# Performance work log

Hardware: AMD Instinct MI355X
Metric: run time of the kernel (lower is better)

The kernel has to match this reference:

```python
import jax, jax.numpy as jnp
import numpy as np

NUM_CENTROIDS = 64
NUM_KMEANS = 5
KM_ITERS = 20


def _kmeans_labels(X, key):
    """Lloyd k-means on X [N,D]; returns final cluster labels [N] (int32).
    Mirrors faiss.Kmeans(dim, num_centroids, niter=...) label assignment."""
    N, D = X.shape
    idx = jax.random.choice(key, N, (NUM_CENTROIDS,), replace=False)
    cent0 = X[idx]  # [C,D] init from random data points

    def assign(cent):
        d = (cent * cent).sum(-1)[None, :] - 2.0 * (X @ cent.T)  # [N,C]
        return jnp.argmin(d, axis=1)

    def step(cent, _):
        lab = assign(cent)
        sums = jax.ops.segment_sum(X, lab, num_segments=NUM_CENTROIDS)  # [C,D]
        cnts = jax.ops.segment_sum(jnp.ones((N,), X.dtype), lab, num_segments=NUM_CENTROIDS)
        newc = jnp.where(cnts[:, None] > 0, sums / jnp.maximum(cnts, 1.0)[:, None], cent)
        return newc, None

    cent, _ = jax.lax.scan(step, cent0, None, length=KM_ITERS)
    return assign(cent)


def setup_inputs() -> dict:
    key = jax.random.key(0)
    k1, k2, k3 = jax.random.split(key, 3)
    N, D = 8192, 512
    adj = jax.random.uniform(k1, (N, N), dtype=jnp.float32)
    student = jax.random.normal(k2, (N, D), dtype=jnp.float32)
    teacher = jax.random.normal(k3, (N, D), dtype=jnp.float32)
    return {"adj": adj, "student": student, "teacher": teacher, "topk": 16}


def reference(adj, student, teacher, topk):
    N, D = student.shape
    # similarity = (student @ teacher.T).detach() + 10*I
    sim = jax.lax.stop_gradient(student @ teacher.T) + 10.0 * jnp.eye(N, dtype=student.dtype)
    _, I_knn = jax.lax.top_k(sim, topk)  # [N, k], sorted descending
    rows = jnp.arange(N)[:, None]  # [N,1]

    # knn_neighbor: sparse ones at (row, I_knn); topk cols are distinct per row
    knn_pat = jnp.zeros((N, N), adj.dtype).at[rows, I_knn].set(1.0)
    locality = knn_pat * adj  # sparse elementwise product knn_neighbor * adj

    # k-means cluster labels over NUM_KMEANS seeds (teacher is detached/cpu in torch)
    Xt = jax.lax.stop_gradient(teacher)
    keys = jax.random.split(jax.random.key(1234), NUM_KMEANS)
    labels = jax.vmap(lambda k: _kmeans_labels(Xt, k))(keys)  # [M,N]

    # close-in-background mask: any seed where label(i) == label(knn_j(i))
    ngh_lab = labels[:, I_knn]               # [M,N,k]
    mask = jnp.any(labels[:, :, None] == ngh_lab, axis=0)  # [N,k]

    # globality: ones at masked (row, knn) positions
    glob_pat = jnp.zeros((N, N), adj.dtype).at[rows, I_knn].add(mask.astype(adj.dtype))

    # pos = locality + globality (dense equivalent of coalesced sparse sum)
    pos = locality + glob_pat
    return pos
```

## Files before the change

kernel.cpp:

```cpp
#include <hip/hip_runtime.h>
#include <stdint.h>

typedef unsigned int u32;
typedef unsigned long long u64;
typedef __attribute__((ext_vector_type(8))) short short8;
typedef __attribute__((ext_vector_type(4))) float f32x4;

#define NN 8192
#define DD 512
#define CC 64
#define RR 5
#define KM_ITERS 20
#define TOPKK 16
#define CHUNK 4096
#define GAP_TH 0.05f
#define FLAGTH 0.02f
#define BAND_TH 0.01f

#define MFMA_BF16 __builtin_amdgcn_mfma_f32_16x16x32_bf16

__device__ __forceinline__ void gload16(void* lds, const void* g) {
  __builtin_amdgcn_global_load_lds(
      (const __attribute__((address_space(1))) void*)g,
      (__attribute__((address_space(3))) void*)lds, 16, 0, 0);
}

__device__ __forceinline__ void tf2x32(u32 k0, u32 k1, u32 x0, u32 x1,
                                       u32& o0, u32& o1) {
  u32 ks2 = k0 ^ k1 ^ 0x1BD11BDAu;
  x0 += k0; x1 += k1;
#define TFR(r) { x0 += x1; x1 = (x1 << r) | (x1 >> (32 - r)); x1 ^= x0; }
  TFR(13) TFR(15) TFR(26) TFR(6)
  x0 += k1; x1 += ks2 + 1u;
  TFR(17) TFR(29) TFR(16) TFR(24)
  x0 += ks2; x1 += k0 + 2u;
  TFR(13) TFR(15) TFR(26) TFR(6)
  x0 += k0; x1 += k1 + 3u;
  TFR(17) TFR(29) TFR(16) TFR(24)
  x0 += k1; x1 += ks2 + 4u;
  TFR(13) TFR(15) TFR(26) TFR(6)
  x0 += ks2; x1 += k0 + 5u;
#undef TFR
  o0 = x0; o1 = x1;
}

__global__ __launch_bounds__(256) void rng_kernel(u32* __restrict__ bits1,
                                                  u32* __restrict__ bits2) {
  int r = blockIdx.x;
  int i = blockIdx.y * 256 + threadIdx.x;
  u32 rk0, rk1; tf2x32(0u, 1234u, 0u, (u32)r, rk0, rk1);
  u32 k10, k11, s10, s11, s20, s21;
  tf2x32(rk0, rk1, 0u, 0u, k10, k11);
  tf2x32(rk0, rk1, 0u, 1u, s10, s11);
  tf2x32(k10, k11, 0u, 1u, s20, s21);
  u32 a, b;
  tf2x32(s10, s11, 0u, (u32)i, a, b);
  bits1[r * NN + i] = a ^ b;
  tf2x32(s20, s21, 0u, (u32)i, a, b);
  bits2[r * NN + i] = a ^ b;
}

__global__ __launch_bounds__(256) void rankpart_kernel(const u32* __restrict__ bits,
                                                       u32* __restrict__ prank) {
  __shared__ u64 sk[2048];
  int r = blockIdx.x, zc = blockIdx.z;
  const u32* bb = bits + (size_t)r * NN;
  int jbase = zc * 2048;
  for (int t = threadIdx.x; t < 2048; t += 256)
    sk[t] = ((u64)bb[jbase + t] << 13) | (u32)(jbase + t);
  __syncthreads();
  int i = blockIdx.y * 256 + threadIdx.x;
  u64 ki = ((u64)bb[i] << 13) | (u32)i;
  int cnt = 0;
#pragma unroll 8
  for (int j = 0; j < 2048; ++j) cnt += (int)(sk[j] < ki);
  prank[(size_t)(r * 4 + zc) * NN + i] = cnt;
}

__global__ __launch_bounds__(256) void scat1_kernel(const u32* __restrict__ prank,
                                                    int* __restrict__ vout) {
  int r = blockIdx.x;
  int i = blockIdx.y * 256 + threadIdx.x;
  int rank = prank[(size_t)(r * 4 + 0) * NN + i] + prank[(size_t)(r * 4 + 1) * NN + i] +
             prank[(size_t)(r * 4 + 2) * NN + i] + prank[(size_t)(r * 4 + 3) * NN + i];
  vout[(size_t)r * NN + rank] = i;
}

__global__ __launch_bounds__(256) void scat2_kernel(const u32* __restrict__ prank,
                                                    const int* __restrict__ v1,
                                                    int* __restrict__ sel) {
  int r = blockIdx.x;
  int i = blockIdx.y * 256 + threadIdx.x;
  int rank = prank[(size_t)(r * 4 + 0) * NN + i] + prank[(size_t)(r * 4 + 1) * NN + i] +
             prank[(size_t)(r * 4 + 2) * NN + i] + prank[(size_t)(r * 4 + 3) * NN + i];
  if (rank < CC) sel[r * CC + rank] = v1[(size_t)r * NN + i];
}

__device__ __forceinline__ double block_reduce_d(double s, double* red4) {
  int tid = threadIdx.x;
  for (int off = 32; off > 0; off >>= 1) s += __shfl_down(s, off, 64);
  if ((tid & 63) == 0) red4[tid >> 6] = s;
  __syncthreads();
  return red4[0] + red4[1] + red4[2] + red4[3];
}

__device__ __forceinline__ u32 bf16rne(float a) {
  u32 ab = __float_as_uint(a);
  return (ab + 0x7FFFu + ((ab >> 16) & 1u)) >> 16;
}
__device__ __forceinline__ void splitf(float a, unsigned short& hi, unsigned short& lo) {
  u32 h = bf16rne(a);
  float hf = __uint_as_float(h << 16);
  hi = (unsigned short)h;
  lo = (unsigned short)bf16rne(a - hf);
}

__global__ __launch_bounds__(256) void init_cent_kernel(const float* __restrict__ X,
                                                        const int* __restrict__ sel,
                                                        double* __restrict__ centD,
                                                        double* __restrict__ cnD,
                                                        float* __restrict__ cnF,
                                                        unsigned short* __restrict__ CHg,
                                                        unsigned short* __restrict__ CLg) {
  __shared__ double red4[4];
  int r = blockIdx.x, c = blockIdx.y, t = threadIdx.x;
  int src = sel[r * CC + c];
  const float* xp = X + (size_t)src * DD;
  size_t o = (size_t)(r * CC + c) * DD;
  double va = (double)xp[t], vb = (double)xp[t + 256];
  centD[o + t] = va; centD[o + t + 256] = vb;
  unsigned short h0, l0, h1, l1;
  splitf((float)va, h0, l0); splitf((float)vb, h1, l1);
  CHg[o + t] = h0; CLg[o + t] = l0;
  CHg[o + t + 256] = h1; CLg[o + t + 256] = l1;
  double tot = block_reduce_d(va * va + vb * vb, red4);
  if (t == 0) { cnD[r * CC + c] = tot; cnF[r * CC + c] = (float)tot; }
}

__global__ __launch_bounds__(256) void split_kernel(const float* __restrict__ in,
                                                    unsigned short* __restrict__ hi,
                                                    unsigned short* __restrict__ lo) {
  size_t base = ((size_t)blockIdx.x * 256 + threadIdx.x) * 8;
  float4 v0 = *(const float4*)(in + base);
  float4 v1 = *(const float4*)(in + base + 4);
  float vv[8] = {v0.x, v0.y, v0.z, v0.w, v1.x, v1.y, v1.z, v1.w};
  unsigned short h[8], l[8];
#pragma unroll
  for (int j = 0; j < 8; ++j) splitf(vv[j], h[j], l[j]);
  uint4 hv, lv;
  hv.x = h[0] | ((u32)h[1] << 16); hv.y = h[2] | ((u32)h[3] << 16);
  hv.z = h[4] | ((u32)h[5] << 16); hv.w = h[6] | ((u32)h[7] << 16);
  lv.x = l[0] | ((u32)l[1] << 16); lv.y = l[2] | ((u32)l[3] << 16);
  lv.z = l[4] | ((u32)l[5] << 16); lv.w = l[6] | ((u32)l[7] << 16);
  *(uint4*)(hi + base) = hv;
  *(uint4*)(lo + base) = lv;
}

__global__ __launch_bounds__(256) void assign_kernel(const unsigned short* __restrict__ XH,
                                                     const unsigned short* __restrict__ XL,
                                                     const unsigned short* __restrict__ CHg,
                                                     const unsigned short* __restrict__ CLg,
                                                     const float* __restrict__ cnF,
                                                     const float* __restrict__ Xf,
                                                     const double* __restrict__ centD,
                                                     const double* __restrict__ cnD,
                                                     int* __restrict__ labels,
                                                     int* __restrict__ bhist,
                                                     int* __restrict__ rib) {
  __shared__ unsigned short Xh[2 * 64 * 32], Xl[2 * 64 * 32],
                            Ch[2 * 64 * 32], Cl[2 * 64 * 32];
  __shared__ float dmat[64 * 68];
  __shared__ int labs[64];
  __shared__ int flagged[64];
  __shared__ int nflag;
  __shared__ double darr[CC];
  __shared__ int h[CC];
  int r = blockIdx.y;
  int blk = blockIdx.x;
  int rowBase = blk * 64;
  int tid = threadIdx.x;
  int wid = tid >> 6, lane = tid & 63, m = lane & 15, q = lane >> 4;
  int srow = wid * 16 + (lane >> 2);
  int sslot = (lane & 3) * 8;
  const unsigned short* gxh = XH + (size_t)(rowBase + srow) * DD + sslot;
  const unsigned short* gxl = XL + (size_t)(rowBase + srow) * DD + sslot;
  const unsigned short* gch = CHg + ((size_t)r * CC + srow) * DD + sslot;
  const unsigned short* gcl = CLg + ((size_t)r * CC + srow) * DD + sslot;
  f32x4 acc[4] = {};
  for (int kc = 0; kc < DD; kc += 64) {
#pragma unroll
    for (int p = 0; p < 2; ++p) {
      int off = p * 2048, ko = kc + p * 32;
      gload16(&Xh[off + wid * 512], gxh + ko);
      gload16(&Xl[off + wid * 512], gxl + ko);
      gload16(&Ch[off + wid * 512], gch + ko);
      gload16(&Cl[off + wid * 512], gcl + ko);
    }
    __syncthreads();
#pragma unroll
    for (int s = 0; s < 2; ++s) {
      int off = s * 2048;
      short8 ah = *(short8*)&Xh[off + (wid * 16 + m) * 32 + q * 8];
      short8 al = *(short8*)&Xl[off + (wid * 16 + m) * 32 + q * 8];
#pragma unroll
      for (int nt = 0; nt < 4; ++nt) {
        short8 bh = *(short8*)&Ch[off + (nt * 16 + m) * 32 + q * 8];
        short8 bl = *(short8*)&Cl[off + (nt * 16 + m) * 32 + q * 8];
        acc[nt] = MFMA_BF16(ah, bh, acc[nt], 0, 0, 0);
        acc[nt] = MFMA_BF16(ah, bl, acc[nt], 0, 0, 0);
        acc[nt] = MFMA_BF16(al, bh, acc[nt], 0, 0, 0);
      }
    }
    __syncthreads();
  }
#pragma unroll
  for (int nt = 0; nt < 4; ++nt) {
    float cn = cnF[r * CC + nt * 16 + m];
#pragma unroll
    for (int reg = 0; reg < 4; ++reg)
      dmat[(wid * 16 + q * 4 + reg) * 68 + nt * 16 + m] = cn - 2.0f * acc[nt][reg];
  }
  if (tid == 0) nflag = 0;
  if (tid < CC) h[tid] = 0;
  __syncthreads();
  if (tid < 64) {
    const float* dr = dmat + (size_t)tid * 68;
    float best = dr[0], second = 3.4e38f; int bi = 0;
    for (int c = 1; c < CC; ++c) {
      float v = dr[c];
      if (v < best) { second = best; best = v; bi = c; }
      else if (v < second) second = v;
    }
    labs[tid] = bi;
    if (second - best < GAP_TH) {
      int s = atomicAdd(&nflag, 1);
      flagged[s] = tid;
    }
  }
  __syncthreads();
  int nf = nflag;
  int cc0 = tid >> 2, sub = tid & 3;
  for (int f = 0; f < nf; ++f) {
    int row = flagged[f];
    const float* x = Xf + (size_t)(rowBase + row) * DD + sub * 128;
    const double* cp = centD + (size_t)(r * CC + cc0) * DD + sub * 128;
    double s = 0.0;
    for (int k = 0; k < 128; ++k) s += (double)x[k] * cp[k];
    s += __shfl_down(s, 2, 64);
    s += __shfl_down(s, 1, 64);
    if (sub == 0) darr[cc0] = cnD[r * CC + cc0] - 2.0 * s;
    __syncthreads();
    if (tid == 0) {
      double best = darr[0]; int bi = 0;
      for (int c2 = 1; c2 < CC; ++c2) { double v = darr[c2]; if (v < best) { best = v; bi = c2; } }
      labs[row] = bi;
    }
    __syncthreads();
  }
  if (tid < 64) {
    int lab = labs[tid];
    atomicAdd(&h[lab], 1);
    int rk = 0;
    for (int j = 0; j < tid; ++j) rk += (labs[j] == lab);
    rib[(size_t)r * NN + rowBase + tid] = rk;
    labels[(size_t)r * NN + rowBase + tid] = lab;
  }
  __syncthreads();
  if (tid < CC) bhist[(size_t)(r * 128 + blk) * CC + tid] = h[tid];
}

__global__ __launch_bounds__(256) void fill_kernel(const int* __restrict__ labels,
                                                   const int* __restrict__ rib,
                                                   const int* __restrict__ bhist,
                                                   int* __restrict__ cstart,
                                                   int* __restrict__ cnt,
                                                   int* __restrict__ member) {
  __shared__ int bh[128 * CC];
  __shared__ int cs[CC];
  __shared__ int tots[CC];
  int r = blockIdx.x, blk = blockIdx.y, tid = threadIdx.x;
  const int* src = bhist + (size_t)r * 128 * CC;
  for (int t = tid; t < 128 * CC; t += 256) bh[t] = src[t];
  __syncthreads();
  if (tid < CC) {
    int run = 0;
    for (int b = 0; b < 128; ++b) { int v = bh[b * CC + tid]; bh[b * CC + tid] = run; run += v; }
    tots[tid] = run;
  }
  __syncthreads();
  if (tid == 0) {
    int run = 0;
    for (int q2 = 0; q2 < CC; ++q2) { cs[q2] = run; run += tots[q2]; }
  }
  __syncthreads();
  int i = blk * 256 + tid;
  int lab = labels[(size_t)r * NN + i];
  int pos = cs[lab] + bh[(i >> 6) * CC + lab] + rib[(size_t)r * NN + i];
  member[(size_t)r * NN + pos] = i;
  if (blk == 0 && tid < CC) { cnt[r * CC + tid] = tots[tid]; cstart[r * CC + tid] = cs[tid]; }
}

__global__ __launch_bounds__(256) void update_kernel(const float* __restrict__ X,
                                                     const int* __restrict__ member,
                                                     const int* __restrict__ cstart,
                                                     const int* __restrict__ cnt,
                                                     const double* __restrict__ centOld,
                                                     double* __restrict__ centNew) {
  __shared__ double part[4][64];
  int r = blockIdx.x, c = blockIdx.y, dchunk = blockIdx.z;
  int tid = threadIdx.x;
  int d = dchunk * 64 + (tid & 63);
  int lane = tid >> 6;
  int n = cnt[r * CC + c];
  int st = cstart[r * CC + c];
  const int* mem = member + (size_t)r * NN + st;
  int n4 = (n + 3) >> 2;
  int lo = lane * n4;
  int hi = min(n, lo + n4);
  double s0 = 0, s1 = 0, s2 = 0, s3 = 0;
  int m = lo;
  for (; m + 3 < hi; m += 4) {
    s0 += (double)X[(size_t)mem[m + 0] * DD + d];
    s1 += (double)X[(size_t)mem[m + 1] * DD + d];
    s2 += (double)X[(size_t)mem[m + 2] * DD + d];
    s3 += (double)X[(size_t)mem[m + 3] * DD + d];
  }
  for (; m < hi; ++m) s0 += (double)X[(size_t)mem[m] * DD + d];
  part[lane][tid & 63] = (s0 + s1) + (s2 + s3);
  __syncthreads();
  if (tid < 64) {
    double tot = (part[0][tid] + part[1][tid]) + (part[2][tid] + part[3][tid]);
    size_t o = (size_t)(r * CC + c) * DD + dchunk * 64 + tid;
    double va = (n > 0) ? tot / (double)n : centOld[o];
    centNew[o] = va;
  }
}

__global__ __launch_bounds__(256) void norm_kernel(const double* __restrict__ centNew,
                                                   double* __restrict__ cnD,
                                                   float* __restrict__ cnF,
                                                   unsigned short* __restrict__ CHg,
                                                   unsigned short* __restrict__ CLg) {
  __shared__ double red4[4];
  int r = blockIdx.x, c = blockIdx.y, t = threadIdx.x;
  size_t o = (size_t)(r * CC + c) * DD;
  double va = centNew[o + t], vb = centNew[o + t + 256];
  unsigned short h0, l0, h1, l1;
  splitf((float)va, h0, l0); splitf((float)vb, h1, l1);
  CHg[o + t] = h0; CLg[o + t] = l0;
  CHg[o + t + 256] = h1; CLg[o + t + 256] = l1;
  double tot = block_reduce_d(va * va + vb * vb, red4);
  if (t == 0) { cnD[r * CC + c] = tot; cnF[r * CC + c] = (float)tot; }
}

__global__ __launch_bounds__(256) void gemm_kernel(const unsigned short* __restrict__ SH,
                                                   const unsigned short* __restrict__ SL,
                                                   const unsigned short* __restrict__ TH,
                                                   const unsigned short* __restrict__ TL,
                                                   float* __restrict__ sim,
                                                   int rowChunk) {
  __shared__ unsigned short Ah[2 * 128 * 32], Al[2 * 128 * 32],
                            Bh[2 * 128 * 32], Bl[2 * 128 * 32];
  int tid = threadIdx.x;
  int wid = tid >> 6, lane = tid & 63, m = lane & 15, q = lane >> 4;
  int waveM = wid >> 1, waveN = wid & 1;
  const int nwgx = NN / 128;
  const int nwg = nwgx * (CHUNK / 128);
  int wg = blockIdx.y * nwgx + blockIdx.x;
  int swz = (wg & 7) * (nwg >> 3) + (wg >> 3);
  int rowTile = swz / nwgx, colTile = swz % nwgx;
  int rowBase = rowChunk + rowTile * 128;
  int colBase = colTile * 128;
  int sr0 = wid * 16 + (lane >> 2);
  int sr1 = (wid + 4) * 16 + (lane >> 2);
  int sslot = (lane & 3) * 8;
  const unsigned short* gah0 = SH + (size_t)(rowBase + sr0) * DD + sslot;
  const unsigned short* gah1 = SH + (size_t)(rowBase + sr1) * DD + sslot;
  const unsigned short* gal0 = SL + (size_t)(rowBase + sr0) * DD + sslot;
  const unsigned short* gal1 = SL + (size_t)(rowBase + sr1) * DD + sslot;
  const unsigned short* gbh0 = TH + (size_t)(colBase + sr0) * DD + sslot;
  const unsigned short* gbh1 = TH + (size_t)(colBase + sr1) * DD + sslot;
  const unsigned short* gbl0 = TL + (size_t)(colBase + sr0) * DD + sslot;
  const unsigned short* gbl1 = TL + (size_t)(colBase + sr1) * DD + sslot;
  f32x4 acc[4][4] = {};
  for (int kc = 0; kc < DD; kc += 64) {
#pragma unroll
    for (int p = 0; p < 2; ++p) {
      int off = p * 4096, ko = kc + p * 32;
      gload16(&Ah[off + wid * 512], gah0 + ko);
      gload16(&Ah[off + (wid + 4) * 512], gah1 + ko);
      gload16(&Al[off + wid * 512], gal0 + ko);
      gload16(&Al[off + (wid + 4) * 512], gal1 + ko);
      gload16(&Bh[off + wid * 512], gbh0 + ko);
      gload16(&Bh[off + (wid + 4) * 512], gbh1 + ko);
      gload16(&Bl[off + wid * 512], gbl0 + ko);
      gload16(&Bl[off + (wid + 4) * 512], gbl1 + ko);
    }
    __syncthreads();
#pragma unroll
    for (int s = 0; s < 2; ++s) {
      int off = s * 4096;
      short8 ah[4], al[4], bh[4], bl[4];
#pragma unroll
      for (int t = 0; t < 4; ++t) {
        ah[t] = *(short8*)&Ah[off + (waveM * 64 + t * 16 + m) * 32 + q * 8];
        al[t] = *(short8*)&Al[off + (waveM * 64 + t * 16 + m) * 32 + q * 8];
        bh[t] = *(short8*)&Bh[off + (waveN * 64 + t * 16 + m) * 32 + q * 8];
        bl[t] = *(short8*)&Bl[off + (waveN * 64 + t * 16 + m) * 32 + q * 8];
      }
#pragma unroll
      for (int mt = 0; mt < 4; ++mt)
#pragma unroll
        for (int nt = 0; nt < 4; ++nt) {
          acc[mt][nt] = MFMA_BF16(ah[mt], bh[nt], acc[mt][nt], 0, 0, 0);
          acc[mt][nt] = MFMA_BF16(ah[mt], bl[nt], acc[mt][nt], 0, 0, 0);
          acc[mt][nt] = MFMA_BF16(al[mt], bh[nt], acc[mt][nt], 0, 0, 0);
        }
    }
    __syncthreads();
  }
#pragma unroll
  for (int mt = 0; mt < 4; ++mt)
#pragma unroll
    for (int nt = 0; nt < 4; ++nt) {
      int gcol = colBase + waveN * 64 + nt * 16 + m;
#pragma unroll
      for (int reg = 0; reg < 4; ++reg) {
        int lrow = rowTile * 128 + waveM * 64 + mt * 16 + q * 4 + reg;
        int grow = rowChunk + lrow;
        float v = acc[mt][nt][reg];
        if (grow == gcol) v += 10.0f;
        sim[(size_t)lrow * NN + gcol] = v;
      }
    }
}

__global__ __launch_bounds__(256) void topk_kernel(const float* __restrict__ sim,
                                                   const float* __restrict__ S,
                                                   const float* __restrict__ T,
                                                   int* __restrict__ iknn,
                                                   int rowChunk) {
  __shared__ u32 rowk[NN];
  __shared__ int bins[4096];
  __shared__ int partial[256];
  __shared__ u64 cand[128];
  __shared__ u64 sure[40];
  __shared__ u64 outk[TOPKK + 1];
  __shared__ u64 red[4];
  __shared__ int nsure, ncand, selB1, selB2, needSel, hardcase;
  __shared__ int nsureR, nbandR;
  __shared__ int sidx[16];
  __shared__ int bidx[64];
  __shared__ double bval[64];

  int blk = blockIdx.x, tid = threadIdx.x;
  int grow = rowChunk + blk;
  const float* rp = sim + (size_t)blk * NN;

  for (int t = tid; t < 4096; t += 256) bins[t] = 0;
  if (tid == 0) { nsure = 0; ncand = 0; hardcase = 0; }
  __syncthreads();
  for (int t = tid; t < NN; t += 256) {
    u32 u = __float_as_uint(rp[t]);
    u = (u & 0x80000000u) ? ~u : (u | 0x80000000u);
    rowk[t] = u;
    atomicAdd(&bins[u >> 20], 1);
  }
  __syncthreads();
  int ps = 0;
#pragma unroll
  for (int b = 0; b < 16; ++b) ps += bins[tid * 16 + b];
  partial[tid] = ps;
  __syncthreads();
  if (tid == 0) {
    int cum = 0, c = 255;
    for (; c > 0; --c) { if (cum + partial[c] >= 17) break; cum += partial[c]; }
    int b = c * 16 + 15;
    for (; b > c * 16; --b) { if (cum + bins[b] >= 17) break; cum += bins[b]; }
    selB1 = b; needSel = 17 - cum;
  }
  __syncthreads();
  int B1 = selB1;
  for (int t = tid; t < NN; t += 256) {
    u32 u = rowk[t];
    int b = (int)(u >> 20);
    if (b < B1) continue;
    u64 key = ((u64)u << 32) | (u32)(NN - 1 - t);
    if (b > B1) { int s = atomicAdd(&nsure, 1); if (s < 40) sure[s] = key; else hardcase = 1; }
    else        { int s = atomicAdd(&ncand, 1); if (s < 128) cand[s] = key; }
  }
  __syncthreads();
  if (ncand > 128) {
    for (int t = tid; t < 4096; t += 256) bins[t] = 0;
    __syncthreads();
    for (int t = tid; t < NN; t += 256) {
      u32 u = rowk[t];
      if ((int)(u >> 20) == B1) atomicAdd(&bins[(u >> 8) & 0xFFFu], 1);
    }
    __syncthreads();
    int p2 = 0;
#pragma unroll
    for (int b = 0; b < 16; ++b) p2 += bins[tid * 16 + b];
    partial[tid] = p2;
    __syncthreads();
    if (tid == 0) {
      int need = needSel;
      int cum = 0, c = 255;
      for (; c > 0; --c) { if (cum + partial[c] >= need) break; cum += partial[c]; }
      int b = c * 16 + 15;
      for (; b > c * 16; --b) { if (cum + bins[b] >= need) break; cum += bins[b]; }
      selB2 = b; ncand = 0;
    }
    __syncthreads();
    int B2 = selB2;
    for (int t = tid; t < NN; t += 256) {
      u32 u = rowk[t];
      if ((int)(u >> 20) != B1) continue;
      int sb = (int)((u >> 8) & 0xFFFu);
      if (sb < B2) continue;
      u64 key = ((u64)u << 32) | (u32)(NN - 1 - t);
      if (sb > B2) { int s = atomicAdd(&nsure, 1); if (s < 40) sure[s] = key; else hardcase = 1; }
      else         { int s = atomicAdd(&ncand, 1); if (s < 128) cand[s] = key; }
    }
    __syncthreads();
    if (tid == 0 && ncand > 128) hardcase = 1;
    __syncthreads();
  }
  if (!hardcase) {
    int ns = nsure, nc = ncand;
    int total = ns + nc;
    if (tid < total) {
      u64 k = tid < ns ? sure[tid] : cand[tid - ns];
      int rank = 0;
      for (int j = 0; j < total; ++j) {
        u64 o = j < ns ? sure[j] : cand[j - ns];
        rank += (int)(o > k);
      }
      if (rank < TOPKK + 1) outk[rank] = k;
    }
  } else {
    for (int k = 0; k < TOPKK + 1; ++k) {
      u64 best = 0;
      for (int t = tid; t < NN; t += 256) {
        u64 key = ((u64)rowk[t] << 32) | (u32)(NN - 1 - t);
        best = key > best ? key : best;
      }
      for (int off = 32; off > 0; off >>= 1) {
        u32 lo = (u32)best, hi = (u32)(best >> 32);
        lo = __shfl_down(lo, off, 64); hi = __shfl_down(hi, off, 64);
        u64 o = ((u64)hi << 32) | lo;
        best = o > best ? o : best;
      }
      if ((tid & 63) == 0) red[tid >> 6] = best;
      __syncthreads();
      if (tid == 0) {
        u64 b = red[0];
        for (int w = 1; w < 4; ++w) b = red[w] > b ? red[w] : b;
        outk[k] = b;
        rowk[(NN - 1) - (int)(b & 0xFFFFFFFFu)] = 0;
      }
      __syncthreads();
    }
  }
  __syncthreads();
  if (hardcase && tid < TOPKK + 1) {
    u64 k = outk[tid];
    rowk[(NN - 1) - (int)(k & 0xFFFFFFFFu)] = (u32)(k >> 32);
  }
  __syncthreads();
  if (tid < TOPKK)
    iknn[(size_t)grow * TOPKK + tid] = (NN - 1) - (int)(outk[tid] & 0xFFFFFFFFu);
  u32 ub16 = (u32)(outk[TOPKK - 1] >> 32), ub17 = (u32)(outk[TOPKK] >> 32);
  float v16 = (ub16 & 0x80000000u) ? __uint_as_float(ub16 & 0x7FFFFFFFu)
                                   : __uint_as_float(~ub16);
  float v17 = (ub17 & 0x80000000u) ? __uint_as_float(ub17 & 0x7FFFFFFFu)
                                   : __uint_as_float(~ub17);
  if (v16 - v17 >= FLAGTH) return;

  if (tid == 0) { nsureR = 0; nbandR = 0; }
  __syncthreads();
  for (int j = tid; j < NN; j += 256) {
    u32 u = rowk[j];
    float v = (u & 0x80000000u) ? __uint_as_float(u & 0x7FFFFFFFu)
                                : __uint_as_float(~u);
    if (v > v16 + BAND_TH) {
      int s = atomicAdd(&nsureR, 1);
      if (s < 16) sidx[s] = j;
    } else if (v >= v16 - BAND_TH) {
      int s = atomicAdd(&nbandR, 1);
      if (s < 64) bidx[s] = j;
    }
  }
  __syncthreads();
  int nb = nbandR > 64 ? 64 : nbandR;
  if (tid < nb) {
    const float* sp = S + (size_t)grow * DD;
    const float* tp = T + (size_t)bidx[tid] * DD;
    double s = 0.0;
    for (int k = 0; k < DD; ++k) s += (double)sp[k] * (double)tp[k];
    bval[tid] = s;
  }
  __syncthreads();
  if (tid == 0) {
    int w = 0;
    int ns = nsureR < 16 ? nsureR : 16;
    for (int i2 = 0; i2 < ns; ++i2) iknn[(size_t)grow * TOPKK + w++] = sidx[i2];
    u64 used = 0;
    while (w < TOPKK) {
      int bj = -1; double bv = 0.0;
      for (int i2 = 0; i2 < nb; ++i2) {
        if (used & (1ull << i2)) continue;
        if (bj < 0 || bval[i2] > bv ||
            (bval[i2] == bv && bidx[i2] < bidx[bj])) { bv = bval[i2]; bj = i2; }
      }
      if (bj < 0) break;
      used |= 1ull << bj;
      iknn[(size_t)grow * TOPKK + w++] = bidx[bj];
    }
  }
}

__global__ __launch_bounds__(256) void zero_kernel(float4* __restrict__ out) {
  size_t i = (size_t)blockIdx.x * 256 + threadIdx.x;
  out[i] = make_float4(0.f, 0.f, 0.f, 0.f);
}

__global__ __launch_bounds__(256) void scatter_kernel(const float* __restrict__ adj,
                                                      const int* __restrict__ iknn,
                                                      const int* __restrict__ labels,
                                                      float* __restrict__ out) {
  int idx = blockIdx.x * 256 + threadIdx.x;
  int i = idx >> 4;
  int col = iknn[idx];
  int m = 0;
#pragma unroll
  for (int r = 0; r < RR; ++r)
    m |= (labels[(size_t)r * NN + i] == labels[(size_t)r * NN + col]);
  size_t o = (size_t)i * NN + col;
  out[o] = adj[o] + (float)m;
}

extern "C" void kernel_launch(void* const* d_in, const int* in_sizes, int n_in,
                              void* d_out, int out_size, void* d_ws, size_t ws_size,
                              hipStream_t stream) {
  (void)in_sizes; (void)n_in; (void)out_size; (void)ws_size;
  const float* adj     = (const float*)d_in[0];
  const float* student = (const float*)d_in[1];
  const float* teacher = (const float*)d_in[2];
  float* out = (float*)d_out;

  char* p = (char*)d_ws;
  auto alloc = [&](size_t bytes) -> void* {
    void* q = (void*)p; p += (bytes + 255) & ~(size_t)255; return q;
  };
  double* centA  = (double*)alloc((size_t)RR * CC * DD * 8);
  double* centB  = (double*)alloc((size_t)RR * CC * DD * 8);
  double* cnD    = (double*)alloc((size_t)RR * CC * 8);
  float*  cnF    = (float*) alloc((size_t)RR * CC * 4);
  u32*    bits1  = (u32*)   alloc((size_t)RR * NN * 4);
  u32*    bits2  = (u32*)   alloc((size_t)RR * NN * 4);
  u32*    prank  = (u32*)   alloc((size_t)RR * 4 * NN * 4);
  int*    v1     = (int*)   alloc((size_t)RR * NN * 4);
  int*    sel    = (int*)   alloc((size_t)RR * CC * 4);
  int*    labels = (int*)   alloc((size_t)RR * NN * 4);
  int*    bhist  = (int*)   alloc((size_t)RR * 128 * CC * 4);
  int*    cstart = (int*)   alloc((size_t)RR * CC * 4);
  int*    cnt    = (int*)   alloc((size_t)RR * CC * 4);
  int*    rib    = (int*)   alloc((size_t)RR * NN * 4);
  int*    member = (int*)   alloc((size_t)RR * NN * 4);
  int*    iknn   = (int*)   alloc((size_t)NN * TOPKK * 4);
  unsigned short* SH = (unsigned short*)alloc((size_t)NN * DD * 2);
  unsigned short* SL = (unsigned short*)alloc((size_t)NN * DD * 2);
  unsigned short* THi = (unsigned short*)alloc((size_t)NN * DD * 2);
  unsigned short* TLo = (unsigned short*)alloc((size_t)NN * DD * 2);
  unsigned short* CHg = (unsigned short*)alloc((size_t)RR * CC * DD * 2);
  unsigned short* CLg = (unsigned short*)alloc((size_t)RR * CC * DD * 2);
  float*  simc   = (float*) alloc((size_t)CHUNK * NN * 4);

  rng_kernel<<<dim3(RR, 32), 256, 0, stream>>>(bits1, bits2);
  rankpart_kernel<<<dim3(RR, 32, 4), 256, 0, stream>>>(bits1, prank);
  scat1_kernel<<<dim3(RR, 32), 256, 0, stream>>>(prank, v1);
  rankpart_kernel<<<dim3(RR, 32, 4), 256, 0, stream>>>(bits2, prank);
  scat2_kernel<<<dim3(RR, 32), 256, 0, stream>>>(prank, v1, sel);
  init_cent_kernel<<<dim3(RR, CC), 256, 0, stream>>>(teacher, sel, centA, cnD, cnF, CHg, CLg);

  split_kernel<<<(NN * DD / 8) / 256, 256, 0, stream>>>(student, SH, SL);
  split_kernel<<<(NN * DD / 8) / 256, 256, 0, stream>>>(teacher, THi, TLo);

  double* cur = centA; double* nxt = centB;
  for (int it = 0; it < KM_ITERS; ++it) {
    assign_kernel<<<dim3(NN / 64, RR), 256, 0, stream>>>(THi, TLo, CHg, CLg, cnF,
                                                         teacher, cur, cnD,
                                                         labels, bhist, rib);
    fill_kernel<<<dim3(RR, 32), 256, 0, stream>>>(labels, rib, bhist, cstart, cnt, member);
    update_kernel<<<dim3(RR, CC, 8), 256, 0, stream>>>(teacher, member, cstart, cnt, cur, nxt);
    norm_kernel<<<dim3(RR, CC), 256, 0, stream>>>(nxt, cnD, cnF, CHg, CLg);
    double* t = cur; cur = nxt; nxt = t;
  }
  assign_kernel<<<dim3(NN / 64, RR), 256, 0, stream>>>(THi, TLo, CHg, CLg, cnF,
                                                       teacher, cur, cnD,
                                                       labels, bhist, rib);

  for (int ch = 0; ch < NN / CHUNK; ++ch) {
    gemm_kernel<<<dim3(NN / 128, CHUNK / 128), 256, 0, stream>>>(SH, SL, THi, TLo, simc,
                                                                 ch * CHUNK);
    topk_kernel<<<CHUNK, 256, 0, stream>>>(simc, student, teacher, iknn, ch * CHUNK);
  }

  zero_kernel<<<(unsigned)((size_t)NN * NN / 4 / 256), 256, 0, stream>>>((float4*)out);
  scatter_kernel<<<NN * TOPKK / 256, 256, 0, stream>>>(adj, iknn, labels, out);
}
```

Baseline: 2.915 ms.

## Move fp64 k-means fixup to a global work-list kernel and unchunk similarity GEMM

The assign kernel no longer runs the fp64 recheck of near-tie rows inline, where each block serially looped over its flagged rows with barriers. It now appends flagged (seed,row) ids to a global list through an atomic counter. A separate fixup kernel spreads that list across 1024 blocks, and a new hist kernel computes the per-block histograms and ranks. The similarity GEMM+topk is also run as one 8192-wide chunk instead of two. This adds several kernel launches per iteration and doubles the similarity buffer size.

```diff
diff --git a/kernel.cpp b/kernel.cpp
--- a/kernel.cpp
+++ b/kernel.cpp
@@ -12,10 +12,11 @@
 #define RR 5
 #define KM_ITERS 20
 #define TOPKK 16
-#define CHUNK 4096
+#define CHUNK 8192
 #define GAP_TH 0.05f
 #define FLAGTH 0.02f
 #define BAND_TH 0.01f
+#define FIXCAP (RR * NN)
 
 #define MFMA_BF16 __builtin_amdgcn_mfma_f32_16x16x32_bf16
 
@@ -161,20 +162,12 @@
                                                      const unsigned short* __restrict__ CHg,
                                                      const unsigned short* __restrict__ CLg,
                                                      const float* __restrict__ cnF,
-                                                     const float* __restrict__ Xf,
-                                                     const double* __restrict__ centD,
-                                                     const double* __restrict__ cnD,
                                                      int* __restrict__ labels,
-                                                     int* __restrict__ bhist,
-                                                     int* __restrict__ rib) {
+                                                     u32* __restrict__ flags,
+                                                     u32* __restrict__ counter) {
   __shared__ unsigned short Xh[2 * 64 * 32], Xl[2 * 64 * 32],
                             Ch[2 * 64 * 32], Cl[2 * 64 * 32];
   __shared__ float dmat[64 * 68];
-  __shared__ int labs[64];
-  __shared__ int flagged[64];
-  __shared__ int nflag;
-  __shared__ double darr[CC];
-  __shared__ int h[CC];
   int r = blockIdx.y;
   int blk = blockIdx.x;
   int rowBase = blk * 64;
@@ -220,8 +213,6 @@
     for (int reg = 0; reg < 4; ++reg)
       dmat[(wid * 16 + q * 4 + reg) * 68 + nt * 16 + m] = cn - 2.0f * acc[nt][reg];
   }
-  if (tid == 0) nflag = 0;
-  if (tid < CC) h[tid] = 0;
   __syncthreads();
   if (tid < 64) {
     const float* dr = dmat + (size_t)tid * 68;
@@ -231,42 +222,59 @@
       if (v < best) { second = best; best = v; bi = c; }
       else if (v < second) second = v;
     }
-    labs[tid] = bi;
+    labels[(size_t)r * NN + rowBase + tid] = bi;
     if (second - best < GAP_TH) {
-      int s = atomicAdd(&nflag, 1);
-      flagged[s] = tid;
-    }
-  }
-  __syncthreads();
-  int nf = nflag;
-  int cc0 = tid >> 2, sub = tid & 3;
-  for (int f = 0; f < nf; ++f) {
-    int row = flagged[f];
-    const float* x = Xf + (size_t)(rowBase + row) * DD + sub * 128;
-    const double* cp = centD + (size_t)(r * CC + cc0) * DD + sub * 128;
+      u32 idx = atomicAdd(counter, 1u);
+      if (idx < FIXCAP) flags[idx] = (u32)(r * NN + rowBase + tid);
+    }
+  }
+}
+
+__global__ __launch_bounds__(256) void fixup_kernel(const float* __restrict__ X,
+                                                    const double* __restrict__ centD,
+                                                    const double* __restrict__ cnD,
+                                                    const u32* __restrict__ flags,
+                                                    const u32* __restrict__ counter,
+                                                    int* __restrict__ labels) {
+  __shared__ double darr[CC];
+  int n = (int)*counter; if (n > FIXCAP) n = FIXCAP;
+  int tid = threadIdx.x, c = tid >> 2, sub = tid & 3;
+  for (int f = blockIdx.x; f < n; f += gridDim.x) {
+    u32 pk = flags[f];
+    int r = pk >> 13, i = pk & (NN - 1);
+    const float* x = X + (size_t)i * DD + sub * 128;
+    const double* cp = centD + (size_t)(r * CC + c) * DD + sub * 128;
     double s = 0.0;
     for (int k = 0; k < 128; ++k) s += (double)x[k] * cp[k];
     s += __shfl_down(s, 2, 64);
     s += __shfl_down(s, 1, 64);
-    if (sub == 0) darr[cc0] = cnD[r * CC + cc0] - 2.0 * s;
+    if (sub == 0) darr[c] = cnD[r * CC + c] - 2.0 * s;
     __syncthreads();
     if (tid == 0) {
       double best = darr[0]; int bi = 0;
-      for (int c2 = 1; c2 < CC; ++c2) { double v = darr[c2]; if (v < best) { best = v; bi = c2; } }
-      labs[row] = bi;
-    }
-    __syncthreads();
-  }
-  if (tid < 64) {
-    int lab = labs[tid];
-    atomicAdd(&h[lab], 1);
-    int rk = 0;
-    for (int j = 0; j < tid; ++j) rk += (labs[j] == lab);
-    rib[(size_t)r * NN + rowBase + tid] = rk;
-    labels[(size_t)r * NN + rowBase + tid] = lab;
-  }
-  __syncthreads();
-  if (tid < CC) bhist[(size_t)(r * 128 + blk) * CC + tid] = h[tid];
+      for (int cc = 1; cc < CC; ++cc) { double v = darr[cc]; if (v < best) { best = v; bi = cc; } }
+      labels[(size_t)r * NN + i] = bi;
+    }
+    __syncthreads();
+  }
+}
+
+__global__ __launch_bounds__(64) void hist_kernel(const int* __restrict__ labels,
+                                                  int* __restrict__ bhist,
+                                                  int* __restrict__ rib) {
+  __shared__ int labs[64];
+  __shared__ int h[CC];
+  int r = blockIdx.y, blk = blockIdx.x, tid = threadIdx.x;
+  labs[tid] = labels[(size_t)r * NN + blk * 64 + tid];
+  h[tid] = 0;
+  __syncthreads();
+  int lab = labs[tid];
+  atomicAdd(&h[lab], 1);
+  int rk = 0;
+  for (int j = 0; j < tid; ++j) rk += (labs[j] == lab);
+  rib[(size_t)r * NN + blk * 64 + tid] = rk;
+  __syncthreads();
+  bhist[(size_t)(r * 128 + blk) * CC + tid] = h[tid];
 }
 
 __global__ __launch_bounds__(256) void fill_kernel(const int* __restrict__ labels,
@@ -625,6 +633,10 @@
   out[i] = make_float4(0.f, 0.f, 0.f, 0.f);
 }
 
+__global__ void zeroc_kernel(u32* __restrict__ c) {
+  c[threadIdx.x] = 0u;
+}
+
 __global__ __launch_bounds__(256) void scatter_kernel(const float* __restrict__ adj,
                                                       const int* __restrict__ iknn,
                                                       const int* __restrict__ labels,
@@ -668,6 +680,8 @@
   int*    cnt    = (int*)   alloc((size_t)RR * CC * 4);
   int*    rib    = (int*)   alloc((size_t)RR * NN * 4);
   int*    member = (int*)   alloc((size_t)RR * NN * 4);
+  u32*    flags  = (u32*)   alloc((size_t)FIXCAP * 4);
+  u32*    counters = (u32*) alloc((size_t)64 * 4);
   int*    iknn   = (int*)   alloc((size_t)NN * TOPKK * 4);
   unsigned short* SH = (unsigned short*)alloc((size_t)NN * DD * 2);
   unsigned short* SL = (unsigned short*)alloc((size_t)NN * DD * 2);
@@ -677,6 +691,8 @@
   unsigned short* CLg = (unsigned short*)alloc((size_t)RR * CC * DD * 2);
   float*  simc   = (float*) alloc((size_t)CHUNK * NN * 4);
 
+  zeroc_kernel<<<1, 64, 0, stream>>>(counters);
+
   rng_kernel<<<dim3(RR, 32), 256, 0, stream>>>(bits1, bits2);
   rankpart_kernel<<<dim3(RR, 32, 4), 256, 0, stream>>>(bits1, prank);
   scat1_kernel<<<dim3(RR, 32), 256, 0, stream>>>(prank, v1);
@@ -690,22 +706,21 @@
   double* cur = centA; double* nxt = centB;
   for (int it = 0; it < KM_ITERS; ++it) {
     assign_kernel<<<dim3(NN / 64, RR), 256, 0, stream>>>(THi, TLo, CHg, CLg, cnF,
-                                                         teacher, cur, cnD,
-                                                         labels, bhist, rib);
+                                                         labels, flags, counters + it);
+    fixup_kernel<<<1024, 256, 0, stream>>>(teacher, cur, cnD, flags, counters + it, labels);
+    hist_kernel<<<dim3(128, RR), 64, 0, stream>>>(labels, bhist, rib);
     fill_kernel<<<dim3(RR, 32), 256, 0, stream>>>(labels, rib, bhist, cstart, cnt, member);
     update_kernel<<<dim3(RR, CC, 8), 256, 0, stream>>>(teacher, member, cstart, cnt, cur, nxt);
     norm_kernel<<<dim3(RR, CC), 256, 0, stream>>>(nxt, cnD, cnF, CHg, CLg);
     double* t = cur; cur = nxt; nxt = t;
   }
   assign_kernel<<<dim3(NN / 64, RR), 256, 0, stream>>>(THi, TLo, CHg, CLg, cnF,
-                                                       teacher, cur, cnD,
-                                                       labels, bhist, rib);
-
-  for (int ch = 0; ch < NN / CHUNK; ++ch) {
-    gemm_kernel<<<dim3(NN / 128, CHUNK / 128), 256, 0, stream>>>(SH, SL, THi, TLo, simc,
-                                                                 ch * CHUNK);
-    topk_kernel<<<CHUNK, 256, 0, stream>>>(simc, student, teacher, iknn, ch * CHUNK);
-  }
+                                                       labels, flags, counters + KM_ITERS);
+  fixup_kernel<<<1024, 256, 0, stream>>>(teacher, cur, cnD, flags,
+                                         counters + KM_ITERS, labels);
+
+  gemm_kernel<<<dim3(NN / 128, CHUNK / 128), 256, 0, stream>>>(SH, SL, THi, TLo, simc, 0);
+  topk_kernel<<<CHUNK, 256, 0, stream>>>(simc, student, teacher, iknn, 0);
 
   zero_kernel<<<(unsigned)((size_t)NN * NN / 4 / 256), 256, 0, stream>>>((float4*)out);
   scatter_kernel<<<NN * TOPKK / 256, 256, 0, stream>>>(adj, iknn, labels, out);
```

New measurement: 2.699 ms. -7.4%, faster.
